# Kernel tuning notes

Hardware: AMD Instinct MI355X
Metric: run time of the kernel (lower is better)

## Reference

```python
import jax, jax.numpy as jnp
import numpy as np

B, S, D_EMBED, D_HIDDEN = 4, 256, 300, 300
C = 5.0  # frozen tanh-scaling constant


def setup_inputs() -> dict:
    key = jax.random.key(0)
    ks = jax.random.split(key, 8)
    w = 0.05  # ~xavier scale for 300x300
    return {
        "inputs": jax.random.normal(ks[0], (B, S, D_EMBED), jnp.float32),
        "rep_mask": jax.random.randint(ks[1], (B, S), 0, 2, jnp.int32),
        "W_fc": jax.random.normal(ks[2], (D_HIDDEN, D_EMBED), jnp.float32) * w,
        "b_fc": jnp.zeros((D_HIDDEN,), jnp.float32),
        "W1": jax.random.normal(ks[3], (D_HIDDEN, D_HIDDEN), jnp.float32) * w,
        "W2": jax.random.normal(ks[4], (D_HIDDEN, D_HIDDEN), jnp.float32) * w,
        "b1": jnp.zeros((D_HIDDEN,), jnp.float32),
        "W_f1": jax.random.normal(ks[5], (D_HIDDEN, D_HIDDEN), jnp.float32) * w,
        "W_f2": jax.random.normal(ks[6], (D_HIDDEN, D_HIDDEN), jnp.float32) * w,
        "b_f": jnp.zeros((D_HIDDEN,), jnp.float32),
    }


def _disa_fwd(inputs, rep_mask_f, W_fc, b_fc, W1, W2, b1, W_f1, W_f2, b_f):
    n_seq = inputs.shape[1]
    # forward direction mask: attend to strictly later positions (triu, diag=1)
    direct = jnp.triu(jnp.ones((n_seq, n_seq), inputs.dtype), k=1)
    # mask[b,i,j] = rep_mask[b,j] * direct[i,j], shape [B,S,S,1]
    mask = (rep_mask_f[:, None, :] * direct[None]) [..., None]

    rep_map = jax.nn.elu(jnp.einsum('bse,he->bsh', inputs, W_fc) + b_fc)  # [B,S,D]
    dep = jnp.einsum('bsh,gh->bsg', rep_map, W1)   # dependent (token j)
    head = jnp.einsum('bsh,gh->bsg', rep_map, W2)  # head (token i)

    # logits[b,i,j,d]
    logits = C * jnp.tanh((dep[:, None, :, :] + head[:, :, None, :] + b1) / C)

    # hand-rolled masked softmax over dim=2 (j), faithful to original
    masked = logits * mask
    mx = jnp.max(masked, axis=2, keepdims=True)
    exps = jnp.exp(masked - mx) * mask
    sums = jnp.sum(exps, axis=2, keepdims=True)
    sums = sums + (sums == 0).astype(logits.dtype)
    attn = (exps / (sums + 1e-20)) * mask

    attn_result = jnp.sum(attn * rep_map[:, None, :, :], axis=2)  # [B,S,D]

    gate = jax.nn.sigmoid(
        jnp.einsum('bsh,gh->bsg', rep_map, W_f1)
        + jnp.einsum('bsh,gh->bsg', attn_result, W_f2)
        + b_f
    )
    out = gate * rep_map + (1.0 - gate) * attn_result
    return out * rep_mask_f[..., None]


def reference(inputs, rep_mask, W_fc, b_fc, W1, W2, b1, W_f1, W_f2, b_f):
    rep_mask_f = rep_mask.astype(inputs.dtype)
    return _disa_fwd(inputs, rep_mask_f, W_fc, b_fc, W1, W2, b1, W_f1, W_f2, b_f)
```

## Files before the change

kernel.cpp:

```cpp
#include <hip/hip_runtime.h>
#include <hip/hip_bf16.h>

#define Dx 300

#define ED     0
#define HEADF  614400
#define ATTNF  921600
#define U_BASE 1228800
#define REPB   0
#define ATB    327680
#define SYNC_FOFF 2000000

#define AG __HIP_MEMORY_SCOPE_AGENT

typedef __attribute__((ext_vector_type(8))) short short8;
typedef __attribute__((ext_vector_type(4))) float f32x4;

union S8 { unsigned int u[4]; unsigned short s[8]; short8 v; };

__device__ __forceinline__ float bf2f(unsigned short u) {
    union { unsigned int i; float f; } v; v.i = ((unsigned int)u) << 16; return v.f;
}
__device__ __forceinline__ unsigned short f2bf(float x) {
    union { float f; unsigned int i; } u; u.f = x;
    return (unsigned short)((u.i + 0x8000u) >> 16);
}
__device__ __forceinline__ float ldf(const void* p, int idx, int isbf) {
    return isbf ? bf2f(((const unsigned short*)p)[idx]) : ((const float*)p)[idx];
}

__device__ __forceinline__ void load8f(const float* rowp, int kb, int kmax,
                                       int valid, float* x) {
    if (valid && kb + 8 <= kmax) {
        float4 a = *(const float4*)(rowp + kb);
        float4 b = *(const float4*)(rowp + kb + 4);
        x[0]=a.x; x[1]=a.y; x[2]=a.z; x[3]=a.w;
        x[4]=b.x; x[5]=b.y; x[6]=b.z; x[7]=b.w;
    } else {
        #pragma unroll
        for (int j = 0; j < 8; ++j) {
            int k = kb + j;
            x[j] = (valid && k < kmax) ? rowp[k] : 0.f;
        }
    }
}
__device__ __forceinline__ short8 pack8(const float* x) {
    S8 H;
    #pragma unroll
    for (int p = 0; p < 4; ++p) {
        union { float f; unsigned int i; } a, b;
        a.f = x[2*p]; b.f = x[2*p+1];
        H.u[p] = ((a.i + 0x8000u) >> 16) | ((b.i + 0x8000u) & 0xFFFF0000u);
    }
    return H.v;
}
__device__ __forceinline__ short8 load8bf(const unsigned short* rowp, int kb,
                                          int kmax, int valid) {
    S8 R;
    if (valid && kb + 8 <= kmax) {
        ushort4 a = *(const ushort4*)(rowp + kb);
        ushort4 b = *(const ushort4*)(rowp + kb + 4);
        R.s[0]=a.x; R.s[1]=a.y; R.s[2]=a.z; R.s[3]=a.w;
        R.s[4]=b.x; R.s[5]=b.y; R.s[6]=b.z; R.s[7]=b.w;
    } else {
        #pragma unroll
        for (int j = 0; j < 8; ++j) {
            int k = kb + j;
            R.s[j] = (valid && k < kmax) ? rowp[k] : (unsigned short)0;
        }
    }
    return R.v;
}
__device__ __forceinline__ short8 loadB(const void* W, int row, int kb, int isbf,
                                        int valid) {
    if (isbf) return load8bf((const unsigned short*)W + row * 300, kb, 300, valid);
    float t[8];
    load8f((const float*)W + row * 300, kb, 300, valid, t);
    return pack8(t);
}

__device__ __forceinline__ int xcd_id() {
    int x;
    asm volatile("s_getreg_b32 %0, hwreg(HW_REG_XCC_ID)" : "=s"(x));
    return x & 7;
}
__device__ __forceinline__ void spin_ge(int* p, int target) {
    int t = 0;
    while (__hip_atomic_load(p, __ATOMIC_RELAXED, AG) < target) {
        __builtin_amdgcn_s_sleep(1);
        if (++t > 500000) break;
    }
    asm volatile("" ::: "memory");
}


__global__ __launch_bounds__(320, 4) void k_fused(
        const void* __restrict__ Xv, const int* __restrict__ mask,
        const void* __restrict__ Wfc, const void* __restrict__ bfc,
        const void* __restrict__ W1,  const void* __restrict__ W2,
        const void* __restrict__ b1v, const void* __restrict__ Wf1,
        const void* __restrict__ Wf2, const void* __restrict__ bfv,
        float* __restrict__ ws, void* __restrict__ outv) {
    __shared__ int s_isbf, s_meta;
    __shared__ unsigned short vlist[256];
    __shared__ int s_cnt, s_tgt;

    const int tid = threadIdx.x;
    int* S = (int*)(ws + SYNC_FOFF);

    if (tid == 0) {
        const int xid = xcd_id();
        int slot = 1000;
        if (xid < 4)
            slot = __hip_atomic_fetch_add(S + (170 + xid) * 64, 1,
                                          __ATOMIC_RELAXED, AG);
        s_meta = (xid << 20) | (slot < 1000 ? slot : 1000);
    }
    if (tid >= 64 && tid < 128) {
        float v = bf2f(((const unsigned short*)Wfc)[tid - 64]);
        int ok = fabsf(v) < 1.0f;
        unsigned long long bal = __ballot(ok);
        if (tid == 64) s_isbf = (bal == ~0ull) ? 1 : 0;
    }
    __syncthreads();
    const int meta = s_meta;
    const int xid = meta >> 20, li = meta & 0xFFFFF;
    if (xid >= 4 || li >= 80) return;
    const int isbf = s_isbf;
    const int bat = xid;
    const int base = bat * 256;
    unsigned short* U = (unsigned short*)(ws + U_BASE);

    if (tid < 256) {
        const int mt = bat * 16 + li / 5, nt = li % 5;
        const int w = tid >> 6, l = tid & 63;
        const int m0 = mt * 16, lm = l & 15, koff = (l >> 4) * 8;
        const int nrow = nt * 64 + w * 16 + lm;
        const int bval = nrow < 300;
        const int ncl = bval ? nrow : 0;
        f32x4 acc = {0.f, 0.f, 0.f, 0.f};
        if (isbf) {
            const unsigned short* Xp = (const unsigned short*)Xv + (m0 + lm) * 300;
            #pragma unroll
            for (int ks = 0; ks < 10; ++ks) {
                short8 a = load8bf(Xp, ks*32 + koff, 300, 1);
                short8 b = loadB(Wfc, ncl, ks*32 + koff, 1, bval);
                acc = __builtin_amdgcn_mfma_f32_16x16x32_bf16(a, b, acc, 0, 0, 0);
            }
        } else {
            const float* Xp = (const float*)Xv + (m0 + lm) * 300;
            #pragma unroll
            for (int ks = 0; ks < 10; ++ks) {
                float t[8]; load8f(Xp, ks*32 + koff, 300, 1, t);
                short8 a = pack8(t);
                short8 b = loadB(Wfc, ncl, ks*32 + koff, 0, bval);
                acc = __builtin_amdgcn_mfma_f32_16x16x32_bf16(a, b, acc, 0, 0, 0);
            }
        }
        if (bval) {
            float bb = ldf(bfc, nrow, isbf);
            #pragma unroll
            for (int r = 0; r < 4; ++r) {
                int mg = m0 + (l >> 4) * 4 + r;
                float v = acc[r] + bb;
                v = v > 0.f ? v : (__expf(v) - 1.f);
                ws[ED + (mg * 300 + nrow) * 2 + 1] = v;
                U[REPB + mg * 320 + nrow] = f2bf(v);
            }
        } else {
            #pragma unroll
            for (int r = 0; r < 4; ++r) {
                int mg = m0 + (l >> 4) * 4 + r;
                U[REPB + mg * 320 + nrow] = 0;
            }
        }
    }
    __syncthreads();
    if (tid == 0)
        __hip_atomic_fetch_add(S + (bat * 16 + li / 5) * 64, 1,
                               __ATOMIC_RELAXED, AG);

    #pragma unroll
    for (int q = 0; q < 2; ++q) {
        const int u = li + q * 80;
        const int mt = bat * 16 + u / 10, nt10 = u % 10;
        if (tid == 0) spin_ge(S + mt * 64, 5);
        __syncthreads();
        if (tid < 256) {
            const int w = tid >> 6, l = tid & 63;
            const int m0 = mt * 16, lm = l & 15, koff = (l >> 4) * 8;
            const int ng = nt10 * 64 + w * 16 + lm;
            const int wsel = ng < 320;
            const int wrow = wsel ? ng : ng - 320;
            const int bval = wrow < 300;
            const int ncl = bval ? wrow : 0;
            const void* Wsel = wsel ? W1 : W2;
            const unsigned short* ap = U + REPB + (m0 + lm) * 320 + koff;
            f32x4 acc = {0.f, 0.f, 0.f, 0.f};
            #pragma unroll
            for (int ks = 0; ks < 10; ++ks) {
                short8 a = *(const short8*)(ap + ks * 32);
                short8 b = loadB(Wsel, ncl, ks*32 + koff, isbf, bval);
                acc = __builtin_amdgcn_mfma_f32_16x16x32_bf16(a, b, acc, 0, 0, 0);
            }
            if (ng < 300) {
                float bb = ldf(b1v, ng, isbf);
                #pragma unroll
                for (int r = 0; r < 4; ++r) {
                    int mg = m0 + (l >> 4) * 4 + r;
                    ws[ED + (mg * 300 + ng) * 2] = __expf(0.4f * (acc[r] + bb));
                }
            } else if (ng >= 320 && ng < 620) {
                #pragma unroll
                for (int r = 0; r < 4; ++r) {
                    int mg = m0 + (l >> 4) * 4 + r;
                    ws[HEADF + mg * 300 + (ng - 320)] = acc[r];
                }
            }
        }
        __syncthreads();
        if (tid == 0) {
            int old = __hip_atomic_fetch_add(S + (64 + bat) * 64, 1,
                                             __ATOMIC_RELAXED, AG);
            if (old == 159)
                __hip_atomic_store(S + (70 + bat) * 64, 1,
                                   __ATOMIC_RELAXED, AG);
        }
    }

    {
        if (tid < 64) {
            int basec = 0;
            #pragma unroll
            for (int c = 0; c < 4; ++c) {
                const int j = c * 64 + tid;
                const int mv = mask[base + j] != 0;
                unsigned long long bal = __ballot(mv);
                int pos = basec + __popcll(bal & ((1ull << tid) - 1ull));
                if (mv) vlist[pos] = (unsigned short)j;
                basec += __popcll(bal);
            }
            if (tid == 0) s_cnt = basec;
        }
        if (tid == 0) spin_ge(S + (70 + bat) * 64, 1);
        __syncthreads();
        const int cnt = s_cnt;
        #pragma unroll
        for (int q = 0; q < 2; ++q) {
            const int iu = 2 * (li + q * 80);
            if (iu < cnt) {
                const int ia = vlist[iu];
                const int hasB = (iu + 1 < cnt);
                const int ib = hasB ? vlist[iu + 1] : ia;
                const int ga = base + ia, gb = base + ib;
                const int d = tid;
                if (d >= 300) {
                    U[ATB + ga * 320 + d] = 0;
                    if (hasB) U[ATB + gb * 320 + d] = 0;
                } else {
                    const float pwa = __expf(0.4f * ws[HEADF + ga * 300 + d]);
                    const float pwb = __expf(0.4f * ws[HEADF + gb * 300 + d]);
                    const float2* ep2 = ((const float2*)(ws + ED)) + base * Dx + d;
                    float sa = 0.f, ra = 0.f, sb = 0.f, rb = 0.f;
                    if (hasB) {
                        float2 v = ep2[ib * Dx];
                        float ua = fmaf(v.x, pwa, 1.0f);
                        float ea = __expf(-10.0f * __builtin_amdgcn_rcpf(ua));
                        sa += ea; ra = fmaf(ea, v.y, ra);
                    }
                    #pragma unroll 8
                    for (int t = iu + 2; t < cnt; ++t) {
                        const int j = vlist[t];
                        float2 v = ep2[j * Dx];
                        float ua = fmaf(v.x, pwa, 1.0f);
                        float ub = fmaf(v.x, pwb, 1.0f);
                        float ea = __expf(-10.0f * __builtin_amdgcn_rcpf(ua));
                        float eb = __expf(-10.0f * __builtin_amdgcn_rcpf(ub));
                        sa += ea; ra = fmaf(ea, v.y, ra);
                        sb += eb; rb = fmaf(eb, v.y, rb);
                    }
                    const float dena = sa + (sa == 0.f ? 1.f : 0.f) + 1e-20f;
                    const float aa = ra / dena;
                    ws[ATTNF + ga * Dx + d] = aa;
                    U[ATB + ga * 320 + d] = f2bf(aa);
                    if (hasB) {
                        const float denb = sb + (sb == 0.f ? 1.f : 0.f) + 1e-20f;
                        const float ab = rb / denb;
                        ws[ATTNF + gb * Dx + d] = ab;
                        U[ATB + gb * 320 + d] = f2bf(ab);
                    }
                }
                __syncthreads();
                if (tid == 0) {
                    __hip_atomic_fetch_add(S + (100 + (ga >> 4)) * 64, 1,
                                           __ATOMIC_RELAXED, AG);
                    if (hasB)
                        __hip_atomic_fetch_add(S + (100 + (gb >> 4)) * 64, 1,
                                               __ATOMIC_RELAXED, AG);
                }
            }
        }
    }

    {
        const int mt3 = bat * 16 + li / 5, nt3 = li % 5;
        const int m0 = mt3 * 16;
        if (tid < 64) {
            int mv = (tid < 16) ? (mask[m0 + tid] != 0) : 0;
            unsigned long long bal = __ballot(mv);
            if (tid == 0) s_tgt = (int)__popcll(bal);
        }
        __syncthreads();
        const int tgt = s_tgt;
        if (tid == 0 && tgt > 0) spin_ge(S + (100 + mt3) * 64, tgt);
        __syncthreads();
        if (tid < 256) {
            const int w = tid >> 6, l = tid & 63;
            const int lm = l & 15, koff = (l >> 4) * 8;
            const int nrow = nt3 * 64 + w * 16 + lm;
            const int bval = nrow < 300;
            const int ncl = bval ? nrow : 0;
            const unsigned short* a1p = U + REPB + (m0 + lm) * 320 + koff;
            const unsigned short* a2p = U + ATB  + (m0 + lm) * 320 + koff;
            f32x4 acc = {0.f, 0.f, 0.f, 0.f};
            #pragma unroll
            for (int ks = 0; ks < 10; ++ks) {
                short8 a = *(const short8*)(a1p + ks * 32);
                short8 bB = loadB(Wf1, ncl, ks*32 + koff, isbf, bval);
                acc = __builtin_amdgcn_mfma_f32_16x16x32_bf16(a, bB, acc, 0, 0, 0);
            }
            #pragma unroll
            for (int ks = 0; ks < 10; ++ks) {
                short8 a = *(const short8*)(a2p + ks * 32);
                short8 bB = loadB(Wf2, ncl, ks*32 + koff, isbf, bval);
                acc = __builtin_amdgcn_mfma_f32_16x16x32_bf16(a, bB, acc, 0, 0, 0);
            }
            if (bval) {
                float bb = ldf(bfv, nrow, isbf);
                #pragma unroll
                for (int r = 0; r < 4; ++r) {
                    int mg = m0 + (l >> 4) * 4 + r;
                    float res2 = 0.f;
                    if (mask[mg]) {
                        float gp = acc[r] + bb;
                        float gate = 1.0f / (1.0f + __expf(-gp));
                        float rv = ws[ED + (mg * 300 + nrow) * 2 + 1];
                        float av = ws[ATTNF + mg * 300 + nrow];
                        res2 = gate * rv + (1.0f - gate) * av;
                    }
                    if (isbf) ((__hip_bfloat16*)outv)[mg * 300 + nrow] = __float2bfloat16(res2);
                    else      ((float*)outv)[mg * 300 + nrow] = res2;
                }
            }
        }
    }
}

extern "C" void kernel_launch(void* const* d_in, const int* in_sizes, int n_in,
                              void* d_out, int out_size, void* d_ws, size_t ws_size,
                              hipStream_t stream) {
    const void* X   = d_in[0];
    const int*  msk = (const int*)d_in[1];
    const void* Wfc = d_in[2];
    const void* bfc = d_in[3];
    const void* W1  = d_in[4];
    const void* W2  = d_in[5];
    const void* b1  = d_in[6];
    const void* Wf1 = d_in[7];
    const void* Wf2 = d_in[8];
    const void* bfv = d_in[9];
    float* ws = (float*)d_ws;

    hipMemsetAsync((char*)d_ws + (size_t)SYNC_FOFF * sizeof(float), 0, 49152, stream);

    hipLaunchKernelGGL(k_fused, dim3(1024), dim3(320), 0, stream,
                       X, msk, Wfc, bfc, W1, W2, b1, Wf1, Wf2, bfv, ws, d_out);
}
```

Baseline: 137.1 us.

## Split persistent fused kernel into four stage kernels launched in sequence

Replaces the single persistent kernel, which used XCD-based block assignment and global atomic spin-wait flags between stages, with four separate kernels: FC+ELU, W1/W2 projections, masked attention and gated output. Stage ordering now comes from kernel launch boundaries, which also removes the sync-flag memset. This drops the spin-waits and the per-XCD block filtering that discarded most of the 1024 launched blocks. In exchange it adds three extra launch overheads and lets each grid size follow its own stage.

```diff
diff --git a/kernel.cpp b/kernel.cpp
--- a/kernel.cpp
+++ b/kernel.cpp
@@ -9,9 +9,6 @@
 #define U_BASE 1228800
 #define REPB   0
 #define ATB    327680
-#define SYNC_FOFF 2000000
-
-#define AG __HIP_MEMORY_SCOPE_AGENT
 
 typedef __attribute__((ext_vector_type(8))) short short8;
 typedef __attribute__((ext_vector_type(4))) float f32x4;
@@ -79,279 +76,229 @@
     return pack8(t);
 }
 
-__device__ __forceinline__ int xcd_id() {
-    int x;
-    asm volatile("s_getreg_b32 %0, hwreg(HW_REG_XCC_ID)" : "=s"(x));
-    return x & 7;
-}
-__device__ __forceinline__ void spin_ge(int* p, int target) {
-    int t = 0;
-    while (__hip_atomic_load(p, __ATOMIC_RELAXED, AG) < target) {
-        __builtin_amdgcn_s_sleep(1);
-        if (++t > 500000) break;
-    }
-    asm volatile("" ::: "memory");
-}
-
-
-__global__ __launch_bounds__(320, 4) void k_fused(
-        const void* __restrict__ Xv, const int* __restrict__ mask,
-        const void* __restrict__ Wfc, const void* __restrict__ bfc,
-        const void* __restrict__ W1,  const void* __restrict__ W2,
-        const void* __restrict__ b1v, const void* __restrict__ Wf1,
-        const void* __restrict__ Wf2, const void* __restrict__ bfv,
-        float* __restrict__ ws, void* __restrict__ outv) {
-    __shared__ int s_isbf, s_meta;
-    __shared__ unsigned short vlist[256];
-    __shared__ int s_cnt, s_tgt;
-
-    const int tid = threadIdx.x;
-    int* S = (int*)(ws + SYNC_FOFF);
-
-    if (tid == 0) {
-        const int xid = xcd_id();
-        int slot = 1000;
-        if (xid < 4)
-            slot = __hip_atomic_fetch_add(S + (170 + xid) * 64, 1,
-                                          __ATOMIC_RELAXED, AG);
-        s_meta = (xid << 20) | (slot < 1000 ? slot : 1000);
-    }
-    if (tid >= 64 && tid < 128) {
-        float v = bf2f(((const unsigned short*)Wfc)[tid - 64]);
+__device__ __forceinline__ int detect_isbf(const void* Wfc, int tid, int* s_isbf) {
+    if (tid < 64) {
+        float v = bf2f(((const unsigned short*)Wfc)[tid]);
         int ok = fabsf(v) < 1.0f;
         unsigned long long bal = __ballot(ok);
-        if (tid == 64) s_isbf = (bal == ~0ull) ? 1 : 0;
+        if (tid == 0) *s_isbf = (bal == ~0ull) ? 1 : 0;
     }
     __syncthreads();
-    const int meta = s_meta;
-    const int xid = meta >> 20, li = meta & 0xFFFFF;
-    if (xid >= 4 || li >= 80) return;
-    const int isbf = s_isbf;
-    const int bat = xid;
+    return *s_isbf;
+}
+
+__global__ __launch_bounds__(256) void k_mm1(
+        const void* __restrict__ Xv, const void* __restrict__ Wfc,
+        const void* __restrict__ bfc, float* __restrict__ ws) {
+    __shared__ int s_isbf;
+    const int tid = threadIdx.x, blk = blockIdx.x;
+    const int isbf = detect_isbf(Wfc, tid, &s_isbf);
+    unsigned short* U = (unsigned short*)(ws + U_BASE);
+    const int bat = (blk & 7) >> 1;
+    const int li  = ((blk >> 3) << 1) | (blk & 1);
+    const int mt = bat * 16 + li / 5, nt = li % 5;
+    const int w = tid >> 6, l = tid & 63;
+    const int m0 = mt * 16, lm = l & 15, koff = (l >> 4) * 8;
+    const int nrow = nt * 64 + w * 16 + lm;
+    const int bval = nrow < 300;
+    const int ncl = bval ? nrow : 0;
+    f32x4 acc = {0.f, 0.f, 0.f, 0.f};
+    if (isbf) {
+        const unsigned short* Xp = (const unsigned short*)Xv + (m0 + lm) * 300;
+        #pragma unroll
+        for (int ks = 0; ks < 10; ++ks) {
+            short8 a = load8bf(Xp, ks*32 + koff, 300, 1);
+            short8 b = loadB(Wfc, ncl, ks*32 + koff, 1, bval);
+            acc = __builtin_amdgcn_mfma_f32_16x16x32_bf16(a, b, acc, 0, 0, 0);
+        }
+    } else {
+        const float* Xp = (const float*)Xv + (m0 + lm) * 300;
+        #pragma unroll
+        for (int ks = 0; ks < 10; ++ks) {
+            float t[8]; load8f(Xp, ks*32 + koff, 300, 1, t);
+            short8 a = pack8(t);
+            short8 b = loadB(Wfc, ncl, ks*32 + koff, 0, bval);
+            acc = __builtin_amdgcn_mfma_f32_16x16x32_bf16(a, b, acc, 0, 0, 0);
+        }
+    }
+    if (bval) {
+        float bb = ldf(bfc, nrow, isbf);
+        #pragma unroll
+        for (int r = 0; r < 4; ++r) {
+            int mg = m0 + (l >> 4) * 4 + r;
+            float v = acc[r] + bb;
+            v = v > 0.f ? v : (__expf(v) - 1.f);
+            ws[ED + (mg * 300 + nrow) * 2 + 1] = v;
+            U[REPB + mg * 320 + nrow] = f2bf(v);
+        }
+    } else {
+        #pragma unroll
+        for (int r = 0; r < 4; ++r) {
+            int mg = m0 + (l >> 4) * 4 + r;
+            U[REPB + mg * 320 + nrow] = 0;
+        }
+    }
+}
+
+__global__ __launch_bounds__(256) void k_mm2(
+        const void* __restrict__ Wfc, const void* __restrict__ W1,
+        const void* __restrict__ W2,  const void* __restrict__ b1v,
+        float* __restrict__ ws) {
+    __shared__ int s_isbf;
+    const int tid = threadIdx.x, blk = blockIdx.x;
+    const int isbf = detect_isbf(Wfc, tid, &s_isbf);
+    const unsigned short* U = (const unsigned short*)(ws + U_BASE);
+    const int bat = (blk & 7) >> 1;
+    const int li  = ((blk >> 3) << 1) | (blk & 1);
+    const int mt = bat * 16 + li / 10, nt10 = li % 10;
+    const int w = tid >> 6, l = tid & 63;
+    const int m0 = mt * 16, lm = l & 15, koff = (l >> 4) * 8;
+    const int ng = nt10 * 64 + w * 16 + lm;
+    const int wsel = ng < 320;
+    const int wrow = wsel ? ng : ng - 320;
+    const int bval = wrow < 300;
+    const int ncl = bval ? wrow : 0;
+    const void* Wsel = wsel ? W1 : W2;
+    const unsigned short* ap = U + REPB + (m0 + lm) * 320 + koff;
+    f32x4 acc = {0.f, 0.f, 0.f, 0.f};
+    #pragma unroll
+    for (int ks = 0; ks < 10; ++ks) {
+        short8 a = *(const short8*)(ap + ks * 32);
+        short8 b = loadB(Wsel, ncl, ks*32 + koff, isbf, bval);
+        acc = __builtin_amdgcn_mfma_f32_16x16x32_bf16(a, b, acc, 0, 0, 0);
+    }
+    if (ng < 300) {
+        float bb = ldf(b1v, ng, isbf);
+        #pragma unroll
+        for (int r = 0; r < 4; ++r) {
+            int mg = m0 + (l >> 4) * 4 + r;
+            ws[ED + (mg * 300 + ng) * 2] = __expf(0.4f * (acc[r] + bb));
+        }
+    } else if (ng >= 320 && ng < 620) {
+        #pragma unroll
+        for (int r = 0; r < 4; ++r) {
+            int mg = m0 + (l >> 4) * 4 + r;
+            ws[HEADF + mg * 300 + (ng - 320)] = acc[r];
+        }
+    }
+}
+
+__global__ __launch_bounds__(320) void k_attn(
+        const int* __restrict__ mask, float* __restrict__ ws) {
+    __shared__ unsigned short vlist[256];
+    __shared__ int s_cnt;
+    const int tid = threadIdx.x, blk = blockIdx.x;
+    unsigned short* U = (unsigned short*)(ws + U_BASE);
+    const int bat = (blk & 7) >> 1;
+    const int li  = ((blk >> 3) << 1) | (blk & 1);
     const int base = bat * 256;
-    unsigned short* U = (unsigned short*)(ws + U_BASE);
-
-    if (tid < 256) {
-        const int mt = bat * 16 + li / 5, nt = li % 5;
-        const int w = tid >> 6, l = tid & 63;
-        const int m0 = mt * 16, lm = l & 15, koff = (l >> 4) * 8;
-        const int nrow = nt * 64 + w * 16 + lm;
-        const int bval = nrow < 300;
-        const int ncl = bval ? nrow : 0;
-        f32x4 acc = {0.f, 0.f, 0.f, 0.f};
-        if (isbf) {
-            const unsigned short* Xp = (const unsigned short*)Xv + (m0 + lm) * 300;
-            #pragma unroll
-            for (int ks = 0; ks < 10; ++ks) {
-                short8 a = load8bf(Xp, ks*32 + koff, 300, 1);
-                short8 b = loadB(Wfc, ncl, ks*32 + koff, 1, bval);
-                acc = __builtin_amdgcn_mfma_f32_16x16x32_bf16(a, b, acc, 0, 0, 0);
+    if (tid < 64) {
+        int basec = 0;
+        #pragma unroll
+        for (int c = 0; c < 4; ++c) {
+            const int j = c * 64 + tid;
+            const int mv = mask[base + j] != 0;
+            unsigned long long bal = __ballot(mv);
+            int pos = basec + __popcll(bal & ((1ull << tid) - 1ull));
+            if (mv) vlist[pos] = (unsigned short)j;
+            basec += __popcll(bal);
+        }
+        if (tid == 0) s_cnt = basec;
+    }
+    __syncthreads();
+    const int cnt = s_cnt;
+    const int iu = 2 * li;
+    if (iu >= cnt) return;
+    const int ia = vlist[iu];
+    const int hasB = (iu + 1 < cnt);
+    const int ib = hasB ? vlist[iu + 1] : ia;
+    const int ga = base + ia, gb = base + ib;
+    const int d = tid;
+    if (d >= 300) {
+        U[ATB + ga * 320 + d] = 0;
+        if (hasB) U[ATB + gb * 320 + d] = 0;
+        return;
+    }
+    const float pwa = __expf(0.4f * ws[HEADF + ga * 300 + d]);
+    const float pwb = __expf(0.4f * ws[HEADF + gb * 300 + d]);
+    const float2* ep2 = ((const float2*)(ws + ED)) + base * Dx + d;
+    float sa = 0.f, ra = 0.f, sb = 0.f, rb = 0.f;
+    if (hasB) {
+        float2 v = ep2[ib * Dx];
+        float ua = fmaf(v.x, pwa, 1.0f);
+        float ea = __expf(-10.0f * __builtin_amdgcn_rcpf(ua));
+        sa += ea; ra = fmaf(ea, v.y, ra);
+    }
+    #pragma unroll 8
+    for (int t = iu + 2; t < cnt; ++t) {
+        const int j = vlist[t];
+        float2 v = ep2[j * Dx];
+        float ua = fmaf(v.x, pwa, 1.0f);
+        float ub = fmaf(v.x, pwb, 1.0f);
+        float ea = __expf(-10.0f * __builtin_amdgcn_rcpf(ua));
+        float eb = __expf(-10.0f * __builtin_amdgcn_rcpf(ub));
+        sa += ea; ra = fmaf(ea, v.y, ra);
+        sb += eb; rb = fmaf(eb, v.y, rb);
+    }
+    const float dena = sa + (sa == 0.f ? 1.f : 0.f) + 1e-20f;
+    const float aa = ra / dena;
+    ws[ATTNF + ga * Dx + d] = aa;
+    U[ATB + ga * 320 + d] = f2bf(aa);
+    if (hasB) {
+        const float denb = sb + (sb == 0.f ? 1.f : 0.f) + 1e-20f;
+        const float ab = rb / denb;
+        ws[ATTNF + gb * Dx + d] = ab;
+        U[ATB + gb * 320 + d] = f2bf(ab);
+    }
+}
+
+__global__ __launch_bounds__(256) void k_mm3(
+        const void* __restrict__ Wfc, const void* __restrict__ Wf1,
+        const void* __restrict__ Wf2, const void* __restrict__ bfv,
+        const int* __restrict__ mask, float* __restrict__ ws,
+        void* __restrict__ outv) {
+    __shared__ int s_isbf;
+    const int tid = threadIdx.x, blk = blockIdx.x;
+    const int isbf = detect_isbf(Wfc, tid, &s_isbf);
+    const unsigned short* U = (const unsigned short*)(ws + U_BASE);
+    const int bat = (blk & 7) >> 1;
+    const int li  = ((blk >> 3) << 1) | (blk & 1);
+    const int mt3 = bat * 16 + li / 5, nt3 = li % 5;
+    const int w = tid >> 6, l = tid & 63;
+    const int m0 = mt3 * 16, lm = l & 15, koff = (l >> 4) * 8;
+    const int nrow = nt3 * 64 + w * 16 + lm;
+    const int bval = nrow < 300;
+    const int ncl = bval ? nrow : 0;
+    const unsigned short* a1p = U + REPB + (m0 + lm) * 320 + koff;
+    const unsigned short* a2p = U + ATB  + (m0 + lm) * 320 + koff;
+    f32x4 acc = {0.f, 0.f, 0.f, 0.f};
+    #pragma unroll
+    for (int ks = 0; ks < 10; ++ks) {
+        short8 a = *(const short8*)(a1p + ks * 32);
+        short8 bB = loadB(Wf1, ncl, ks*32 + koff, isbf, bval);
+        acc = __builtin_amdgcn_mfma_f32_16x16x32_bf16(a, bB, acc, 0, 0, 0);
+    }
+    #pragma unroll
+    for (int ks = 0; ks < 10; ++ks) {
+        short8 a = *(const short8*)(a2p + ks * 32);
+        short8 bB = loadB(Wf2, ncl, ks*32 + koff, isbf, bval);
+        acc = __builtin_amdgcn_mfma_f32_16x16x32_bf16(a, bB, acc, 0, 0, 0);
+    }
+    if (bval) {
+        float bb = ldf(bfv, nrow, isbf);
+        #pragma unroll
+        for (int r = 0; r < 4; ++r) {
+            int mg = m0 + (l >> 4) * 4 + r;
+            float res = 0.f;
+            if (mask[mg]) {
+                float gp = acc[r] + bb;
+                float gate = 1.0f / (1.0f + __expf(-gp));
+                float rv = ws[ED + (mg * 300 + nrow) * 2 + 1];
+                float av = ws[ATTNF + mg * 300 + nrow];
+                res = gate * rv + (1.0f - gate) * av;
             }
-        } else {
-            const float* Xp = (const float*)Xv + (m0 + lm) * 300;
-            #pragma unroll
-            for (int ks = 0; ks < 10; ++ks) {
-                float t[8]; load8f(Xp, ks*32 + koff, 300, 1, t);
-                short8 a = pack8(t);
-                short8 b = loadB(Wfc, ncl, ks*32 + koff, 0, bval);
-                acc = __builtin_amdgcn_mfma_f32_16x16x32_bf16(a, b, acc, 0, 0, 0);
-            }
-        }
-        if (bval) {
-            float bb = ldf(bfc, nrow, isbf);
-            #pragma unroll
-            for (int r = 0; r < 4; ++r) {
-                int mg = m0 + (l >> 4) * 4 + r;
-                float v = acc[r] + bb;
-                v = v > 0.f ? v : (__expf(v) - 1.f);
-                ws[ED + (mg * 300 + nrow) * 2 + 1] = v;
-                U[REPB + mg * 320 + nrow] = f2bf(v);
-            }
-        } else {
-            #pragma unroll
-            for (int r = 0; r < 4; ++r) {
-                int mg = m0 + (l >> 4) * 4 + r;
-                U[REPB + mg * 320 + nrow] = 0;
-            }
-        }
-    }
-    __syncthreads();
-    if (tid == 0)
-        __hip_atomic_fetch_add(S + (bat * 16 + li / 5) * 64, 1,
-                               __ATOMIC_RELAXED, AG);
-
-    #pragma unroll
-    for (int q = 0; q < 2; ++q) {
-        const int u = li + q * 80;
-        const int mt = bat * 16 + u / 10, nt10 = u % 10;
-        if (tid == 0) spin_ge(S + mt * 64, 5);
-        __syncthreads();
-        if (tid < 256) {
-            const int w = tid >> 6, l = tid & 63;
-            const int m0 = mt * 16, lm = l & 15, koff = (l >> 4) * 8;
-            const int ng = nt10 * 64 + w * 16 + lm;
-            const int wsel = ng < 320;
-            const int wrow = wsel ? ng : ng - 320;
-            const int bval = wrow < 300;
-            const int ncl = bval ? wrow : 0;
-            const void* Wsel = wsel ? W1 : W2;
-            const unsigned short* ap = U + REPB + (m0 + lm) * 320 + koff;
-            f32x4 acc = {0.f, 0.f, 0.f, 0.f};
-            #pragma unroll
-            for (int ks = 0; ks < 10; ++ks) {
-                short8 a = *(const short8*)(ap + ks * 32);
-                short8 b = loadB(Wsel, ncl, ks*32 + koff, isbf, bval);
-                acc = __builtin_amdgcn_mfma_f32_16x16x32_bf16(a, b, acc, 0, 0, 0);
-            }
-            if (ng < 300) {
-                float bb = ldf(b1v, ng, isbf);
-                #pragma unroll
-                for (int r = 0; r < 4; ++r) {
-                    int mg = m0 + (l >> 4) * 4 + r;
-                    ws[ED + (mg * 300 + ng) * 2] = __expf(0.4f * (acc[r] + bb));
-                }
-            } else if (ng >= 320 && ng < 620) {
-                #pragma unroll
-                for (int r = 0; r < 4; ++r) {
-                    int mg = m0 + (l >> 4) * 4 + r;
-                    ws[HEADF + mg * 300 + (ng - 320)] = acc[r];
-                }
-            }
-        }
-        __syncthreads();
-        if (tid == 0) {
-            int old = __hip_atomic_fetch_add(S + (64 + bat) * 64, 1,
-                                             __ATOMIC_RELAXED, AG);
-            if (old == 159)
-                __hip_atomic_store(S + (70 + bat) * 64, 1,
-                                   __ATOMIC_RELAXED, AG);
-        }
-    }
-
-    {
-        if (tid < 64) {
-            int basec = 0;
-            #pragma unroll
-            for (int c = 0; c < 4; ++c) {
-                const int j = c * 64 + tid;
-                const int mv = mask[base + j] != 0;
-                unsigned long long bal = __ballot(mv);
-                int pos = basec + __popcll(bal & ((1ull << tid) - 1ull));
-                if (mv) vlist[pos] = (unsigned short)j;
-                basec += __popcll(bal);
-            }
-            if (tid == 0) s_cnt = basec;
-        }
-        if (tid == 0) spin_ge(S + (70 + bat) * 64, 1);
-        __syncthreads();
-        const int cnt = s_cnt;
-        #pragma unroll
-        for (int q = 0; q < 2; ++q) {
-            const int iu = 2 * (li + q * 80);
-            if (iu < cnt) {
-                const int ia = vlist[iu];
-                const int hasB = (iu + 1 < cnt);
-                const int ib = hasB ? vlist[iu + 1] : ia;
-                const int ga = base + ia, gb = base + ib;
-                const int d = tid;
-                if (d >= 300) {
-                    U[ATB + ga * 320 + d] = 0;
-                    if (hasB) U[ATB + gb * 320 + d] = 0;
-                } else {
-                    const float pwa = __expf(0.4f * ws[HEADF + ga * 300 + d]);
-                    const float pwb = __expf(0.4f * ws[HEADF + gb * 300 + d]);
-                    const float2* ep2 = ((const float2*)(ws + ED)) + base * Dx + d;
-                    float sa = 0.f, ra = 0.f, sb = 0.f, rb = 0.f;
-                    if (hasB) {
-                        float2 v = ep2[ib * Dx];
-                        float ua = fmaf(v.x, pwa, 1.0f);
-                        float ea = __expf(-10.0f * __builtin_amdgcn_rcpf(ua));
-                        sa += ea; ra = fmaf(ea, v.y, ra);
-                    }
-                    #pragma unroll 8
-                    for (int t = iu + 2; t < cnt; ++t) {
-                        const int j = vlist[t];
-                        float2 v = ep2[j * Dx];
-                        float ua = fmaf(v.x, pwa, 1.0f);
-                        float ub = fmaf(v.x, pwb, 1.0f);
-                        float ea = __expf(-10.0f * __builtin_amdgcn_rcpf(ua));
-                        float eb = __expf(-10.0f * __builtin_amdgcn_rcpf(ub));
-                        sa += ea; ra = fmaf(ea, v.y, ra);
-                        sb += eb; rb = fmaf(eb, v.y, rb);
-                    }
-                    const float dena = sa + (sa == 0.f ? 1.f : 0.f) + 1e-20f;
-                    const float aa = ra / dena;
-                    ws[ATTNF + ga * Dx + d] = aa;
-                    U[ATB + ga * 320 + d] = f2bf(aa);
-                    if (hasB) {
-                        const float denb = sb + (sb == 0.f ? 1.f : 0.f) + 1e-20f;
-                        const float ab = rb / denb;
-                        ws[ATTNF + gb * Dx + d] = ab;
-                        U[ATB + gb * 320 + d] = f2bf(ab);
-                    }
-                }
-                __syncthreads();
-                if (tid == 0) {
-                    __hip_atomic_fetch_add(S + (100 + (ga >> 4)) * 64, 1,
-                                           __ATOMIC_RELAXED, AG);
-                    if (hasB)
-                        __hip_atomic_fetch_add(S + (100 + (gb >> 4)) * 64, 1,
-                                               __ATOMIC_RELAXED, AG);
-                }
-            }
-        }
-    }
-
-    {
-        const int mt3 = bat * 16 + li / 5, nt3 = li % 5;
-        const int m0 = mt3 * 16;
-        if (tid < 64) {
-            int mv = (tid < 16) ? (mask[m0 + tid] != 0) : 0;
-            unsigned long long bal = __ballot(mv);
-            if (tid == 0) s_tgt = (int)__popcll(bal);
-        }
-        __syncthreads();
-        const int tgt = s_tgt;
-        if (tid == 0 && tgt > 0) spin_ge(S + (100 + mt3) * 64, tgt);
-        __syncthreads();
-        if (tid < 256) {
-            const int w = tid >> 6, l = tid & 63;
-            const int lm = l & 15, koff = (l >> 4) * 8;
-            const int nrow = nt3 * 64 + w * 16 + lm;
-            const int bval = nrow < 300;
-            const int ncl = bval ? nrow : 0;
-            const unsigned short* a1p = U + REPB + (m0 + lm) * 320 + koff;
-            const unsigned short* a2p = U + ATB  + (m0 + lm) * 320 + koff;
-            f32x4 acc = {0.f, 0.f, 0.f, 0.f};
-            #pragma unroll
-            for (int ks = 0; ks < 10; ++ks) {
-                short8 a = *(const short8*)(a1p + ks * 32);
-                short8 bB = loadB(Wf1, ncl, ks*32 + koff, isbf, bval);
-                acc = __builtin_amdgcn_mfma_f32_16x16x32_bf16(a, bB, acc, 0, 0, 0);
-            }
-            #pragma unroll
-            for (int ks = 0; ks < 10; ++ks) {
-                short8 a = *(const short8*)(a2p + ks * 32);
-                short8 bB = loadB(Wf2, ncl, ks*32 + koff, isbf, bval);
-                acc = __builtin_amdgcn_mfma_f32_16x16x32_bf16(a, bB, acc, 0, 0, 0);
-            }
-            if (bval) {
-                float bb = ldf(bfv, nrow, isbf);
-                #pragma unroll
-                for (int r = 0; r < 4; ++r) {
-                    int mg = m0 + (l >> 4) * 4 + r;
-                    float res2 = 0.f;
-                    if (mask[mg]) {
-                        float gp = acc[r] + bb;
-                        float gate = 1.0f / (1.0f + __expf(-gp));
-                        float rv = ws[ED + (mg * 300 + nrow) * 2 + 1];
-                        float av = ws[ATTNF + mg * 300 + nrow];
-                        res2 = gate * rv + (1.0f - gate) * av;
-                    }
-                    if (isbf) ((__hip_bfloat16*)outv)[mg * 300 + nrow] = __float2bfloat16(res2);
-                    else      ((float*)outv)[mg * 300 + nrow] = res2;
-                }
-            }
+            if (isbf) ((__hip_bfloat16*)outv)[mg * 300 + nrow] = __float2bfloat16(res);
+            else      ((float*)outv)[mg * 300 + nrow] = res;
         }
     }
 }
@@ -371,8 +318,9 @@
     const void* bfv = d_in[9];
     float* ws = (float*)d_ws;
 
-    hipMemsetAsync((char*)d_ws + (size_t)SYNC_FOFF * sizeof(float), 0, 49152, stream);
-
-    hipLaunchKernelGGL(k_fused, dim3(1024), dim3(320), 0, stream,
-                       X, msk, Wfc, bfc, W1, W2, b1, Wf1, Wf2, bfv, ws, d_out);
-}
+    hipLaunchKernelGGL(k_mm1,  dim3(320), dim3(256), 0, stream, X, Wfc, bfc, ws);
+    hipLaunchKernelGGL(k_mm2,  dim3(640), dim3(256), 0, stream, Wfc, W1, W2, b1, ws);
+    hipLaunchKernelGGL(k_attn, dim3(512), dim3(320), 0, stream, msk, ws);
+    hipLaunchKernelGGL(k_mm3,  dim3(320), dim3(256), 0, stream,
+                       Wfc, Wf1, Wf2, bfv, msk, ws, d_out);
+}
```

After: 115.6 us. -15.6%, faster.
